# Optimization experiments

Measured on AMD Instinct MI355X. Metric: run time of the kernel, lower is better.

The kernel has to match this reference:

```python
import jax, jax.numpy as jnp
import numpy as np

B, T, C, H = 2, 2048, 1024, 16
HD = C // H  # head dim = 64


def setup_inputs() -> dict:
    key = jax.random.key(0)
    k1, k2, k3 = jax.random.split(key, 3)
    scale = 0.02
    x = jax.random.normal(k1, (B, T, C), dtype=jnp.float32)
    w_attn = jax.random.normal(k2, (C, 3 * C), dtype=jnp.float32) * scale
    b_attn = jnp.zeros((3 * C,), dtype=jnp.float32)
    w_proj = jax.random.normal(k3, (C, C), dtype=jnp.float32) * scale
    b_proj = jnp.zeros((C,), dtype=jnp.float32)
    return {"x": x, "w_attn": w_attn, "b_attn": b_attn, "w_proj": w_proj, "b_proj": b_proj}


def reference(x, w_attn, b_attn, w_proj, b_proj):
    b, t, c = x.shape
    qkv = x @ w_attn + b_attn  # [B,T,3C]
    q, k, v = jnp.split(qkv, 3, axis=-1)
    # [B,T,C] -> [B,H,T,HD]
    q = q.reshape(b, t, H, HD).transpose(0, 2, 1, 3)
    k = k.reshape(b, t, H, HD).transpose(0, 2, 1, 3)
    v = v.reshape(b, t, H, HD).transpose(0, 2, 1, 3)
    att = jnp.einsum('bhqd,bhkd->bhqk', q, k) * (1.0 / jnp.sqrt(jnp.float32(HD)))
    causal = jnp.tril(jnp.ones((t, t), dtype=bool))  # [T,T]
    att = jnp.where(causal[None, None, :, :], att, jnp.float32(-jnp.inf))
    att = jax.nn.softmax(att, axis=-1)
    y = jnp.einsum('bhqk,bhkd->bhqd', att, v)
    y = y.transpose(0, 2, 1, 3).reshape(b, t, c)
    return y @ w_proj + b_proj
```

## Files before the change

### kernel.cpp

```cpp
#include <hip/hip_runtime.h>


typedef unsigned short u16;
typedef unsigned short u16x8 __attribute__((ext_vector_type(8)));
typedef __bf16 bf16x8 __attribute__((ext_vector_type(8)));
typedef float f32x4 __attribute__((ext_vector_type(4)));

#define MFMA16(a, b, c) __builtin_amdgcn_mfma_f32_16x16x32_bf16(a, b, c, 0, 0, 0)

static __device__ __forceinline__ u16 f2b(float f) {
  union { float f; unsigned int i; } x; x.f = f;
  unsigned int r = x.i + 0x7fffu + ((x.i >> 16) & 1u);
  return (u16)(r >> 16);
}
static __device__ __forceinline__ u16 f2b_trunc(float f) {
  union { float f; unsigned int i; } x; x.f = f;
  return (u16)(x.i >> 16);
}

__global__ __launch_bounds__(256) void cast_f32_bf16(
    const float* __restrict__ in, u16* __restrict__ out) {
  int i = (blockIdx.x * 256 + threadIdx.x) * 8;
  float4 a = *(const float4*)&in[i];
  float4 b = *(const float4*)&in[i + 4];
  u16x8 o;
  o[0] = f2b(a.x); o[1] = f2b(a.y); o[2] = f2b(a.z); o[3] = f2b(a.w);
  o[4] = f2b(b.x); o[5] = f2b(b.y); o[6] = f2b(b.z); o[7] = f2b(b.w);
  *(u16x8*)&out[i] = o;
}

__global__ __launch_bounds__(256) void transpose_f32_bf16(
    const float* __restrict__ in, u16* __restrict__ out, int R, int Cc) {
  __shared__ u16 tile[32][33];
  int bx = blockIdx.x, by = blockIdx.y;
  int tx = threadIdx.x, ty = threadIdx.y;
#pragma unroll
  for (int i = 0; i < 4; i++) {
    int r = by * 32 + ty + i * 8;
    int c = bx * 32 + tx;
    tile[ty + i * 8][tx] = f2b(in[r * Cc + c]);
  }
  __syncthreads();
#pragma unroll
  for (int i = 0; i < 4; i++) {
    int r = bx * 32 + ty + i * 8;
    int c = by * 32 + tx;
    out[r * R + c] = tile[tx][ty + i * 8];
  }
}

template <int MODE>
__global__ __launch_bounds__(256, 2) void gemm_bt(
    const u16* __restrict__ A, const u16* __restrict__ Bt,
    const float* __restrict__ bias, float* __restrict__ out,
    u16* __restrict__ Qb, u16* __restrict__ Kb, u16* __restrict__ Vb,
    int M, int N, int K) {
  __shared__ u16 lA[128 * 40];
  __shared__ u16 lB[128 * 40];

  const int tid = threadIdx.x;
  const int lane = tid & 63;
  const int w = tid >> 6;
  const int wm = (w >> 1) * 64, wn = (w & 1) * 64;
  const int l15 = lane & 15, quad = lane >> 4;
  const int m0 = blockIdx.y * 128, n0 = blockIdx.x * 128;

  const int srow = tid >> 2;
  const int scol = (tid & 3) * 8;

  f32x4 acc[4][4] = {};

  for (int k0 = 0; k0 < K; k0 += 32) {
    __syncthreads();
#pragma unroll
    for (int h = 0; h < 2; h++) {
      int r = srow + h * 64;
      *(u16x8*)&lA[r * 40 + scol] = *(const u16x8*)&A[(m0 + r) * K + k0 + scol];
      *(u16x8*)&lB[r * 40 + scol] = *(const u16x8*)&Bt[(n0 + r) * K + k0 + scol];
    }
    __syncthreads();

    bf16x8 af[4], bfr[4];
#pragma unroll
    for (int mi = 0; mi < 4; mi++)
      af[mi] = *(const bf16x8*)&lA[(wm + mi * 16 + l15) * 40 + quad * 8];
#pragma unroll
    for (int ni = 0; ni < 4; ni++)
      bfr[ni] = *(const bf16x8*)&lB[(wn + ni * 16 + l15) * 40 + quad * 8];
#pragma unroll
    for (int mi = 0; mi < 4; mi++)
#pragma unroll
      for (int ni = 0; ni < 4; ni++)
        acc[mi][ni] = MFMA16(af[mi], bfr[ni], acc[mi][ni]);
  }

#pragma unroll
  for (int mi = 0; mi < 4; mi++) {
#pragma unroll
    for (int ni = 0; ni < 4; ni++) {
      int n = n0 + wn + ni * 16 + l15;
      float bv = bias[n];
#pragma unroll
      for (int reg = 0; reg < 4; reg++) {
        int m = m0 + wm + mi * 16 + quad * 4 + reg;
        float v = acc[mi][ni][reg] + bv;
        if (MODE == 1) {
          out[m * N + n] = v;
        } else {
          int which = n >> 10;
          if (which == 1) v *= 0.18033688011112042f;
          int hn = n & 1023;
          int hh = hn >> 6, d = hn & 63;
          int b = m >> 11, t = m & 2047;
          u16* dst = (which == 0) ? Qb : ((which == 1) ? Kb : Vb);
          dst[(((b << 4) + hh) * 2048 + t) * 64 + d] = f2b(v);
        }
      }
    }
  }
}

__global__ __launch_bounds__(256, 4) void attn_kernel(
    const u16* __restrict__ Qg, const u16* __restrict__ Kg,
    const u16* __restrict__ Vg, u16* __restrict__ Yg) {
  __shared__ u16 lk[64 * 72];
  __shared__ u16 lvt[64 * 72];
  __shared__ u16 lp[4][16 * 72];

  const int qt = 31 - blockIdx.x;
  const int bh = blockIdx.y;
  const int tid = threadIdx.x;
  const int lane = tid & 63;
  const int w = tid >> 6;
  const int l15 = lane & 15, quad = lane >> 4;
  const int qbase = qt * 64;
  const int base = bh * 2048 * 64;

  const int sr = tid >> 3;
  const int sc = (tid & 7) * 8;

  const u16* qrow = Qg + base + (qbase + w * 16 + l15) * 64;
  bf16x8 aq0 = *(const bf16x8*)&qrow[quad * 8];
  bf16x8 aq1 = *(const bf16x8*)&qrow[32 + quad * 8];

  u16x8 onesu = {0x3F80, 0x3F80, 0x3F80, 0x3F80, 0x3F80, 0x3F80, 0x3F80, 0x3F80};
  bf16x8 ones = *(const bf16x8*)&onesu;

  const u16* kp = Kg + base;
  const u16* vp = Vg + base;

  u16x8 kr[2], vr[2];
#pragma unroll
  for (int h = 0; h < 2; h++) {
    int r = sr + h * 32;
    kr[h] = *(const u16x8*)&kp[r * 64 + sc];
    vr[h] = *(const u16x8*)&vp[r * 64 + sc];
  }

  f32x4 oacc[4] = {};
  f32x4 lacc = {};

  for (int kt = 0; kt <= qt; kt++) {
    __syncthreads();
#pragma unroll
    for (int h = 0; h < 2; h++) {
      int r = sr + h * 32;
      *(u16x8*)&lk[r * 72 + sc] = kr[h];
      int kvp = r ^ sc;
#pragma unroll
      for (int j = 0; j < 8; j++) lvt[(sc + j) * 72 + kvp] = vr[h][j];
    }
    __syncthreads();
    if (kt < qt) {
      int kvb = (kt + 1) * 64;
#pragma unroll
      for (int h = 0; h < 2; h++) {
        int r = kvb + sr + h * 32;
        kr[h] = *(const u16x8*)&kp[r * 64 + sc];
        vr[h] = *(const u16x8*)&vp[r * 64 + sc];
      }
    }

    f32x4 sa[4] = {};
#pragma unroll
    for (int nt = 0; nt < 4; nt++) {
      bf16x8 bk0 = *(const bf16x8*)&lk[(nt * 16 + l15) * 72 + quad * 8];
      bf16x8 bk1 = *(const bf16x8*)&lk[(nt * 16 + l15) * 72 + 32 + quad * 8];
      sa[nt] = MFMA16(aq0, bk0, sa[nt]);
      sa[nt] = MFMA16(aq1, bk1, sa[nt]);
    }

    const bool diag = (kt == qt);
#pragma unroll
    for (int nt = 0; nt < 4; nt++) {
      int kcol = nt * 16 + l15;
#pragma unroll
      for (int reg = 0; reg < 4; reg++) {
        float s = sa[nt][reg];
        if (diag) {
          int qr = w * 16 + quad * 4 + reg;
          if (kcol > qr) s = -1e30f;
        }
        lp[w][(quad * 4 + reg) * 72 + nt * 16 + l15] = f2b_trunc(exp2f(s));
      }
    }

    bf16x8 pa0 = *(const bf16x8*)&lp[w][l15 * 72 + quad * 8];
    bf16x8 pa1 = *(const bf16x8*)&lp[w][l15 * 72 + 32 + quad * 8];

    lacc = MFMA16(pa0, ones, lacc);
    lacc = MFMA16(pa1, ones, lacc);
#pragma unroll
    for (int dt = 0; dt < 4; dt++) {
      int d = dt * 16 + l15;
      int dsw = d & 56;
      bf16x8 bv0 = *(const bf16x8*)&lvt[d * 72 + ((quad * 8) ^ dsw)];
      bf16x8 bv1 = *(const bf16x8*)&lvt[d * 72 + ((32 + quad * 8) ^ dsw)];
      oacc[dt] = MFMA16(pa0, bv0, oacc[dt]);
      oacc[dt] = MFMA16(pa1, bv1, oacc[dt]);
    }
  }

  const int b = bh >> 4, hh = bh & 15;
  float inv[4];
#pragma unroll
  for (int reg = 0; reg < 4; reg++) inv[reg] = 1.0f / lacc[reg];
#pragma unroll
  for (int dt = 0; dt < 4; dt++)
#pragma unroll
    for (int reg = 0; reg < 4; reg++) {
      int q = qbase + w * 16 + quad * 4 + reg;
      int col = hh * 64 + dt * 16 + l15;
      Yg[(b * 2048 + q) * 1024 + col] = f2b(oacc[dt][reg] * inv[reg]);
    }
}

extern "C" void kernel_launch(void* const* d_in, const int* in_sizes, int n_in,
                              void* d_out, int out_size, void* d_ws, size_t ws_size,
                              hipStream_t stream) {
  const float* x      = (const float*)d_in[0];
  const float* w_attn = (const float*)d_in[1];
  const float* b_attn = (const float*)d_in[2];
  const float* w_proj = (const float*)d_in[3];
  const float* b_proj = (const float*)d_in[4];
  float* out = (float*)d_out;

  char* ws = (char*)d_ws;
  u16* wattnT = (u16*)(ws);
  u16* wprojT = (u16*)(ws + 6291456);
  u16* xb     = (u16*)(ws + 8388608);
  u16* Qb     = (u16*)(ws + 16777216);
  u16* Kb     = (u16*)(ws + 25165824);
  u16* Vb     = (u16*)(ws + 33554432);
  u16* Yb     = (u16*)(ws + 41943040);

  cast_f32_bf16<<<2048, 256, 0, stream>>>(x, xb);
  transpose_f32_bf16<<<dim3(96, 32), dim3(32, 8), 0, stream>>>(w_attn, wattnT, 1024, 3072);
  transpose_f32_bf16<<<dim3(32, 32), dim3(32, 8), 0, stream>>>(w_proj, wprojT, 1024, 1024);
  gemm_bt<0><<<dim3(24, 32), 256, 0, stream>>>(xb, wattnT, b_attn, nullptr,
                                               Qb, Kb, Vb, 4096, 3072, 1024);
  attn_kernel<<<dim3(32, 32), 256, 0, stream>>>(Qb, Kb, Vb, Yb);
  gemm_bt<1><<<dim3(8, 32), 256, 0, stream>>>(Yb, wprojT, b_proj, out,
                                              nullptr, nullptr, nullptr, 4096, 1024, 1024);
}
```

Baseline: 226.0 us.

## Load attention K/V fragments directly from global memory, pre-transpose V

Removes the LDS staging of K and V tiles and both per-iteration __syncthreads in the attention kernel; each wave now loads its MFMA B-operand fragments straight from global memory (relying on L2/L1 for reuse across the 4 waves). A new transpose_v kernel writes V in [bh][d][t] layout into the no-longer-needed xb buffer so V fragments are contiguous. This trades LDS traffic and barriers for redundant global/cache reads per wave, loses the register prefetch of the next tile, and adds an extra kernel with strided scalar writes.

```diff
diff --git a/kernel.cpp b/kernel.cpp
--- a/kernel.cpp
+++ b/kernel.cpp
@@ -46,6 +46,20 @@
     int r = bx * 32 + ty + i * 8;
     int c = by * 32 + tx;
     out[r * R + c] = tile[tx][ty + i * 8];
+  }
+}
+
+__global__ __launch_bounds__(256) void transpose_v(
+    const u16* __restrict__ in, u16* __restrict__ out) {
+  int bh = blockIdx.y;
+  int t = blockIdx.x * 128 + (threadIdx.x & 127);
+  int dg = (threadIdx.x >> 7) * 32;
+  const u16* src = in + (bh * 2048 + t) * 64;
+  u16* dst = out + bh * 64 * 2048 + t;
+#pragma unroll
+  for (int i = 0; i < 32; i++) {
+    int d = dg + i;
+    dst[d * 2048] = src[d];
   }
 }
 
@@ -122,9 +136,7 @@
 
 __global__ __launch_bounds__(256, 4) void attn_kernel(
     const u16* __restrict__ Qg, const u16* __restrict__ Kg,
-    const u16* __restrict__ Vg, u16* __restrict__ Yg) {
-  __shared__ u16 lk[64 * 72];
-  __shared__ u16 lvt[64 * 72];
+    const u16* __restrict__ Vt, u16* __restrict__ Yg) {
   __shared__ u16 lp[4][16 * 72];
 
   const int qt = 31 - blockIdx.x;
@@ -135,9 +147,7 @@
   const int l15 = lane & 15, quad = lane >> 4;
   const int qbase = qt * 64;
   const int base = bh * 2048 * 64;
-
-  const int sr = tid >> 3;
-  const int sc = (tid & 7) * 8;
+  const int vbase = bh * 64 * 2048;
 
   const u16* qrow = Qg + base + (qbase + w * 16 + l15) * 64;
   bf16x8 aq0 = *(const bf16x8*)&qrow[quad * 8];
@@ -146,48 +156,36 @@
   u16x8 onesu = {0x3F80, 0x3F80, 0x3F80, 0x3F80, 0x3F80, 0x3F80, 0x3F80, 0x3F80};
   bf16x8 ones = *(const bf16x8*)&onesu;
 
-  const u16* kp = Kg + base;
-  const u16* vp = Vg + base;
-
-  u16x8 kr[2], vr[2];
-#pragma unroll
-  for (int h = 0; h < 2; h++) {
-    int r = sr + h * 32;
-    kr[h] = *(const u16x8*)&kp[r * 64 + sc];
-    vr[h] = *(const u16x8*)&vp[r * 64 + sc];
-  }
+  const u16* kfb = Kg + base + l15 * 64 + quad * 8;
+  const u16* vfb = Vt + vbase + l15 * 2048 + quad * 8;
+
+  u16* lpw = &lp[w][0];
 
   f32x4 oacc[4] = {};
   f32x4 lacc = {};
 
   for (int kt = 0; kt <= qt; kt++) {
-    __syncthreads();
-#pragma unroll
-    for (int h = 0; h < 2; h++) {
-      int r = sr + h * 32;
-      *(u16x8*)&lk[r * 72 + sc] = kr[h];
-      int kvp = r ^ sc;
-#pragma unroll
-      for (int j = 0; j < 8; j++) lvt[(sc + j) * 72 + kvp] = vr[h][j];
-    }
-    __syncthreads();
-    if (kt < qt) {
-      int kvb = (kt + 1) * 64;
-#pragma unroll
-      for (int h = 0; h < 2; h++) {
-        int r = kvb + sr + h * 32;
-        kr[h] = *(const u16x8*)&kp[r * 64 + sc];
-        vr[h] = *(const u16x8*)&vp[r * 64 + sc];
-      }
+    const int kvb = kt * 64;
+
+    bf16x8 bk[4][2], bv[4][2];
+#pragma unroll
+    for (int nt = 0; nt < 4; nt++) {
+      const u16* p = kfb + (kvb + nt * 16) * 64;
+      bk[nt][0] = *(const bf16x8*)&p[0];
+      bk[nt][1] = *(const bf16x8*)&p[32];
+    }
+#pragma unroll
+    for (int dt = 0; dt < 4; dt++) {
+      const u16* p = vfb + dt * 16 * 2048 + kvb;
+      bv[dt][0] = *(const bf16x8*)&p[0];
+      bv[dt][1] = *(const bf16x8*)&p[32];
     }
 
     f32x4 sa[4] = {};
 #pragma unroll
     for (int nt = 0; nt < 4; nt++) {
-      bf16x8 bk0 = *(const bf16x8*)&lk[(nt * 16 + l15) * 72 + quad * 8];
-      bf16x8 bk1 = *(const bf16x8*)&lk[(nt * 16 + l15) * 72 + 32 + quad * 8];
-      sa[nt] = MFMA16(aq0, bk0, sa[nt]);
-      sa[nt] = MFMA16(aq1, bk1, sa[nt]);
+      sa[nt] = MFMA16(aq0, bk[nt][0], sa[nt]);
+      sa[nt] = MFMA16(aq1, bk[nt][1], sa[nt]);
     }
 
     const bool diag = (kt == qt);
@@ -201,23 +199,19 @@
           int qr = w * 16 + quad * 4 + reg;
           if (kcol > qr) s = -1e30f;
         }
-        lp[w][(quad * 4 + reg) * 72 + nt * 16 + l15] = f2b_trunc(exp2f(s));
+        lpw[(quad * 4 + reg) * 72 + nt * 16 + l15] = f2b_trunc(exp2f(s));
       }
     }
 
-    bf16x8 pa0 = *(const bf16x8*)&lp[w][l15 * 72 + quad * 8];
-    bf16x8 pa1 = *(const bf16x8*)&lp[w][l15 * 72 + 32 + quad * 8];
+    bf16x8 pa0 = *(const bf16x8*)&lpw[l15 * 72 + quad * 8];
+    bf16x8 pa1 = *(const bf16x8*)&lpw[l15 * 72 + 32 + quad * 8];
 
     lacc = MFMA16(pa0, ones, lacc);
     lacc = MFMA16(pa1, ones, lacc);
 #pragma unroll
     for (int dt = 0; dt < 4; dt++) {
-      int d = dt * 16 + l15;
-      int dsw = d & 56;
-      bf16x8 bv0 = *(const bf16x8*)&lvt[d * 72 + ((quad * 8) ^ dsw)];
-      bf16x8 bv1 = *(const bf16x8*)&lvt[d * 72 + ((32 + quad * 8) ^ dsw)];
-      oacc[dt] = MFMA16(pa0, bv0, oacc[dt]);
-      oacc[dt] = MFMA16(pa1, bv1, oacc[dt]);
+      oacc[dt] = MFMA16(pa0, bv[dt][0], oacc[dt]);
+      oacc[dt] = MFMA16(pa1, bv[dt][1], oacc[dt]);
     }
   }
 
@@ -249,6 +243,7 @@
   u16* wattnT = (u16*)(ws);
   u16* wprojT = (u16*)(ws + 6291456);
   u16* xb     = (u16*)(ws + 8388608);
+  u16* Vt     = xb;
   u16* Qb     = (u16*)(ws + 16777216);
   u16* Kb     = (u16*)(ws + 25165824);
   u16* Vb     = (u16*)(ws + 33554432);
@@ -259,7 +254,8 @@
   transpose_f32_bf16<<<dim3(32, 32), dim3(32, 8), 0, stream>>>(w_proj, wprojT, 1024, 1024);
   gemm_bt<0><<<dim3(24, 32), 256, 0, stream>>>(xb, wattnT, b_attn, nullptr,
                                                Qb, Kb, Vb, 4096, 3072, 1024);
-  attn_kernel<<<dim3(32, 32), 256, 0, stream>>>(Qb, Kb, Vb, Yb);
+  transpose_v<<<dim3(16, 32), 256, 0, stream>>>(Vb, Vt);
+  attn_kernel<<<dim3(32, 32), 256, 0, stream>>>(Qb, Kb, Vt, Yb);
   gemm_bt<1><<<dim3(8, 32), 256, 0, stream>>>(Yb, wprojT, b_proj, out,
                                               nullptr, nullptr, nullptr, 4096, 1024, 1024);
 }
```

Result: slower. 381.5 us (+68.8%).

## Pre-transpose V in global memory to avoid scalar LDS transposes in attention

Applied to the files above, without the earlier changes.

Adds a separate kernel that transposes V into a [bh, d, t] layout, written into the no-longer-needed xb buffer, so the attention kernel can store V tiles to shared memory with vector writes instead of eight scalar swizzled writes per thread. The P·V operand reads drop the XOR swizzle. The cost is an extra kernel launch and an extra pass over V in global memory. The transpose kernel's stores are 2-byte scalars, coalesced across t, which may limit its bandwidth.

```diff
diff --git a/kernel.cpp b/kernel.cpp
--- a/kernel.cpp
+++ b/kernel.cpp
@@ -46,6 +46,20 @@
     int r = bx * 32 + ty + i * 8;
     int c = by * 32 + tx;
     out[r * R + c] = tile[tx][ty + i * 8];
+  }
+}
+
+__global__ __launch_bounds__(256) void transpose_v(
+    const u16* __restrict__ in, u16* __restrict__ out) {
+  int bh = blockIdx.y;
+  int t = blockIdx.x * 128 + (threadIdx.x & 127);
+  int dg = (threadIdx.x >> 7) * 32;
+  const u16* src = in + (bh * 2048 + t) * 64;
+  u16* dst = out + bh * 64 * 2048 + t;
+#pragma unroll
+  for (int i = 0; i < 32; i++) {
+    int d = dg + i;
+    dst[d * 2048] = src[d];
   }
 }
 
@@ -122,7 +136,7 @@
 
 __global__ __launch_bounds__(256, 4) void attn_kernel(
     const u16* __restrict__ Qg, const u16* __restrict__ Kg,
-    const u16* __restrict__ Vg, u16* __restrict__ Yg) {
+    const u16* __restrict__ Vt, u16* __restrict__ Yg) {
   __shared__ u16 lk[64 * 72];
   __shared__ u16 lvt[64 * 72];
   __shared__ u16 lp[4][16 * 72];
@@ -135,6 +149,7 @@
   const int l15 = lane & 15, quad = lane >> 4;
   const int qbase = qt * 64;
   const int base = bh * 2048 * 64;
+  const int vbase = bh * 64 * 2048;
 
   const int sr = tid >> 3;
   const int sc = (tid & 7) * 8;
@@ -147,16 +162,17 @@
   bf16x8 ones = *(const bf16x8*)&onesu;
 
   const u16* kp = Kg + base;
-  const u16* vp = Vg + base;
+  const u16* vp = Vt + vbase;
 
   u16x8 kr[2], vr[2];
 #pragma unroll
   for (int h = 0; h < 2; h++) {
     int r = sr + h * 32;
     kr[h] = *(const u16x8*)&kp[r * 64 + sc];
-    vr[h] = *(const u16x8*)&vp[r * 64 + sc];
-  }
-
+    vr[h] = *(const u16x8*)&vp[r * 2048 + sc];
+  }
+
+  u16* lpw = &lp[w][0];
   f32x4 oacc[4] = {};
   f32x4 lacc = {};
 
@@ -166,18 +182,16 @@
     for (int h = 0; h < 2; h++) {
       int r = sr + h * 32;
       *(u16x8*)&lk[r * 72 + sc] = kr[h];
-      int kvp = r ^ sc;
-#pragma unroll
-      for (int j = 0; j < 8; j++) lvt[(sc + j) * 72 + kvp] = vr[h][j];
+      *(u16x8*)&lvt[r * 72 + sc] = vr[h];
     }
     __syncthreads();
     if (kt < qt) {
       int kvb = (kt + 1) * 64;
 #pragma unroll
       for (int h = 0; h < 2; h++) {
-        int r = kvb + sr + h * 32;
-        kr[h] = *(const u16x8*)&kp[r * 64 + sc];
-        vr[h] = *(const u16x8*)&vp[r * 64 + sc];
+        int r = sr + h * 32;
+        kr[h] = *(const u16x8*)&kp[(kvb + r) * 64 + sc];
+        vr[h] = *(const u16x8*)&vp[r * 2048 + kvb + sc];
       }
     }
 
@@ -201,21 +215,19 @@
           int qr = w * 16 + quad * 4 + reg;
           if (kcol > qr) s = -1e30f;
         }
-        lp[w][(quad * 4 + reg) * 72 + nt * 16 + l15] = f2b_trunc(exp2f(s));
+        lpw[(quad * 4 + reg) * 72 + nt * 16 + l15] = f2b_trunc(exp2f(s));
       }
     }
 
-    bf16x8 pa0 = *(const bf16x8*)&lp[w][l15 * 72 + quad * 8];
-    bf16x8 pa1 = *(const bf16x8*)&lp[w][l15 * 72 + 32 + quad * 8];
+    bf16x8 pa0 = *(const bf16x8*)&lpw[l15 * 72 + quad * 8];
+    bf16x8 pa1 = *(const bf16x8*)&lpw[l15 * 72 + 32 + quad * 8];
 
     lacc = MFMA16(pa0, ones, lacc);
     lacc = MFMA16(pa1, ones, lacc);
 #pragma unroll
     for (int dt = 0; dt < 4; dt++) {
-      int d = dt * 16 + l15;
-      int dsw = d & 56;
-      bf16x8 bv0 = *(const bf16x8*)&lvt[d * 72 + ((quad * 8) ^ dsw)];
-      bf16x8 bv1 = *(const bf16x8*)&lvt[d * 72 + ((32 + quad * 8) ^ dsw)];
+      bf16x8 bv0 = *(const bf16x8*)&lvt[(dt * 16 + l15) * 72 + quad * 8];
+      bf16x8 bv1 = *(const bf16x8*)&lvt[(dt * 16 + l15) * 72 + 32 + quad * 8];
       oacc[dt] = MFMA16(pa0, bv0, oacc[dt]);
       oacc[dt] = MFMA16(pa1, bv1, oacc[dt]);
     }
@@ -249,6 +261,7 @@
   u16* wattnT = (u16*)(ws);
   u16* wprojT = (u16*)(ws + 6291456);
   u16* xb     = (u16*)(ws + 8388608);
+  u16* Vt     = xb;
   u16* Qb     = (u16*)(ws + 16777216);
   u16* Kb     = (u16*)(ws + 25165824);
   u16* Vb     = (u16*)(ws + 33554432);
@@ -259,7 +272,8 @@
   transpose_f32_bf16<<<dim3(32, 32), dim3(32, 8), 0, stream>>>(w_proj, wprojT, 1024, 1024);
   gemm_bt<0><<<dim3(24, 32), 256, 0, stream>>>(xb, wattnT, b_attn, nullptr,
                                                Qb, Kb, Vb, 4096, 3072, 1024);
-  attn_kernel<<<dim3(32, 32), 256, 0, stream>>>(Qb, Kb, Vb, Yb);
+  transpose_v<<<dim3(16, 32), 256, 0, stream>>>(Vb, Vt);
+  attn_kernel<<<dim3(32, 32), 256, 0, stream>>>(Qb, Kb, Vt, Yb);
   gemm_bt<1><<<dim3(8, 32), 256, 0, stream>>>(Yb, wprojT, b_proj, out,
                                               nullptr, nullptr, nullptr, 4096, 1024, 1024);
 }
```

New measurement: 224.8 us. About the same (-0.5%).
